# Kernel optimization log

Measured on AMD Instinct MI355X. Metric: run time of the kernel, lower is better.

Reference implementation:

```python
import jax, jax.numpy as jnp
import numpy as np

EPS = 1e-5
GROUPS = 8

def group_norm(x, gamma, beta):
    # x: [B,C,H,W], 8 groups
    B, C, H, W = x.shape
    xg = x.reshape(B, GROUPS, C // GROUPS, H, W)
    mu = jnp.mean(xg, axis=(2, 3, 4), keepdims=True)
    var = jnp.mean((xg - mu) ** 2, axis=(2, 3, 4), keepdims=True)
    xn = ((xg - mu) * jax.lax.rsqrt(var + EPS)).reshape(B, C, H, W)
    return xn * gamma[None, :, None, None] + beta[None, :, None, None]

def setup_inputs() -> dict:
    key = jax.random.key(0)
    ks = jax.random.split(key, 7)
    B, C, H, W = 4, 256, 64, 64
    x = jax.random.normal(ks[0], (B, C, H, W), dtype=jnp.float32)
    gamma = jnp.ones((C,), dtype=jnp.float32)
    beta = jnp.zeros((C,), dtype=jnp.float32)
    s = 1.0 / np.sqrt(C)
    w_qkv = jax.random.normal(ks[1], (3 * C, C), dtype=jnp.float32) * s
    b_qkv = jnp.zeros((3 * C,), dtype=jnp.float32)
    w_proj = jax.random.normal(ks[2], (C, C), dtype=jnp.float32) * s
    b_proj = jnp.zeros((C,), dtype=jnp.float32)
    return {"x": x, "gamma": gamma, "beta": beta, "w_qkv": w_qkv,
            "b_qkv": b_qkv, "w_proj": w_proj, "b_proj": b_proj}

def reference(x, gamma, beta, w_qkv, b_qkv, w_proj, b_proj):
    B, C, H, W = x.shape
    N = H * W
    h = group_norm(x, gamma, beta)
    # 1x1 conv == per-pixel matmul
    qkv = jnp.einsum('bchw,oc->bohw', h, w_qkv) + b_qkv[None, :, None, None]
    q, k, v = jnp.split(qkv, 3, axis=1)  # each [B,C,H,W]
    q = q.reshape(B, C, N).transpose(0, 2, 1)   # [B,N,C]
    k = k.reshape(B, C, N)                      # [B,C,N]
    v = v.reshape(B, C, N).transpose(0, 2, 1)   # [B,N,C]
    attn = jax.nn.softmax(jnp.einsum('bnc,bcm->bnm', q, k) / jnp.sqrt(jnp.float32(C)), axis=-1)
    out = jnp.einsum('bnm,bmc->bnc', attn, v)   # [B,N,C]
    out = out.transpose(0, 2, 1).reshape(B, C, H, W)
    proj = jnp.einsum('bchw,oc->bohw', out, w_proj) + b_proj[None, :, None, None]
    return x + proj
```

## Files before the change

### kernel.cpp

```cpp
#include <hip/hip_runtime.h>
#include <hip/hip_bf16.h>
#include <math.h>

#define B 4
#define C 256
#define G 8
#define N 4096
#define EPSV 1e-5f
#define SCALE 0.0625f

typedef __attribute__((ext_vector_type(8))) short short8;
typedef __attribute__((ext_vector_type(16))) float f32x16;
typedef unsigned short ushort_t;
typedef unsigned int uint_t;

__device__ __forceinline__ ushort_t f2bf(float f) {
    union { float f; uint_t u; } c; c.f = f;
    uint_t u = c.u;
    uint_t r = (u + 0x7FFFu + ((u >> 16) & 1u)) >> 16;
    return (ushort_t)r;
}
__device__ __forceinline__ float bf2f(ushort_t h) {
    union { uint_t u; float f; } c; c.u = ((uint_t)h) << 16;
    return c.f;
}
__device__ __forceinline__ uint_t pack2(float a, float b) {
    return (uint_t)f2bf(a) | ((uint_t)f2bf(b) << 16);
}
__device__ __forceinline__ uint_t cvtpk_bf16(float lo, float hi) {
    uint_t r;
    asm("v_cvt_pk_bf16_f32 %0, %1, %2" : "=v"(r) : "v"(lo), "v"(hi));
    return r;
}
__device__ __forceinline__ void gl_lds16(const void* g, void* l) {
    __builtin_amdgcn_global_load_lds(
        (const __attribute__((address_space(1))) void*)g,
        (__attribute__((address_space(3))) void*)l, 16, 0, 0);
}

__global__ __launch_bounds__(256) void wconv(const float* __restrict__ wq,
        const float* __restrict__ wp, ushort_t* __restrict__ wbf) {
    int idx = blockIdx.x*256 + threadIdx.x;
    #pragma unroll
    for (int p = 0; p < 4; p++) {
        int id = idx + p*16384;
        float4 v = (id < 49152) ? ((const float4*)wq)[id] : ((const float4*)wp)[id - 49152];
        uint2 pk; pk.x = pack2(v.x, v.y); pk.y = pack2(v.z, v.w);
        *(uint2*)&wbf[(size_t)id*4] = pk;
    }
}

__global__ __launch_bounds__(256) void gn_partial(const float* __restrict__ x,
                                                  float* __restrict__ partials) {
    int blk = blockIdx.x;
    int bg = blk >> 3;
    int part = blk & 7;
    const float4* xp4 = (const float4*)(x + (size_t)bg * (32 * N) + (size_t)part * (32 * N / 8));
    float s = 0.f, ss = 0.f;
    for (int i = threadIdx.x; i < 4096; i += 256) {
        float4 v = xp4[i];
        s  += v.x + v.y + v.z + v.w;
        ss += v.x*v.x + v.y*v.y + v.z*v.z + v.w*v.w;
    }
    __shared__ float rs[256], rss[256];
    rs[threadIdx.x] = s; rss[threadIdx.x] = ss;
    __syncthreads();
    for (int off = 128; off > 0; off >>= 1) {
        if (threadIdx.x < off) {
            rs[threadIdx.x]  += rs[threadIdx.x + off];
            rss[threadIdx.x] += rss[threadIdx.x + off];
        }
        __syncthreads();
    }
    if (threadIdx.x == 0) {
        partials[(bg*8 + part)*2]     = rs[0];
        partials[(bg*8 + part)*2 + 1] = rss[0];
    }
}

__global__ void gn_final(const float* __restrict__ partials, float* __restrict__ stats) {
    int t = threadIdx.x;
    if (t < 32) {
        float s = 0.f, ss = 0.f;
        for (int p = 0; p < 8; p++) {
            s  += partials[(t*8 + p)*2];
            ss += partials[(t*8 + p)*2 + 1];
        }
        const float inv = 1.f / 131072.f;
        float mu = s * inv;
        float var = fmaxf(ss * inv - mu*mu, 0.f);
        stats[t*2]     = mu;
        stats[t*2 + 1] = rsqrtf(var + EPSV);
    }
}

__global__ __launch_bounds__(256) void norm_bf16(const float* __restrict__ x,
        const float* __restrict__ gamma, const float* __restrict__ beta,
        const float* __restrict__ stats, ushort_t* __restrict__ hbf) {
    int b = blockIdx.z, c0 = blockIdx.y*64, n0 = blockIdx.x*64;
    int t = threadIdx.x;
    int cq = t >> 4, nq = t & 15;
    ushort_t hv[4][4];
    #pragma unroll
    for (int i = 0; i < 4; i++) {
        int c = c0 + cq*4 + i;
        int g = c >> 5;
        float mu = stats[(b*G+g)*2], rs = stats[(b*G+g)*2+1];
        float ga = gamma[c]*rs;
        float be = beta[c] - mu*ga;
        float4 v = *(const float4*)&x[((size_t)(b*C + c))*N + n0 + nq*4];
        hv[i][0] = f2bf(v.x*ga + be);
        hv[i][1] = f2bf(v.y*ga + be);
        hv[i][2] = f2bf(v.z*ga + be);
        hv[i][3] = f2bf(v.w*ga + be);
    }
    #pragma unroll
    for (int j = 0; j < 4; j++) {
        uint2 pk;
        pk.x = (uint_t)hv[0][j] | ((uint_t)hv[1][j]<<16);
        pk.y = (uint_t)hv[2][j] | ((uint_t)hv[3][j]<<16);
        *(uint2*)&hbf[((size_t)(b*N + n0 + nq*4 + j))*256 + c0 + cq*4] = pk;
    }
}

__global__ __launch_bounds__(256) void qkv_mfma(const ushort_t* __restrict__ hbf,
        const ushort_t* __restrict__ wbf, const float* __restrict__ bias,
        ushort_t* __restrict__ qbf, ushort_t* __restrict__ kbf, ushort_t* __restrict__ vblk) {
    int b = blockIdx.z, o0 = blockIdx.y*128, n0 = blockIdx.x*128;
    int tid = threadIdx.x;
    int w = tid>>6, l = tid&63, l31 = l&31, lh = l>>5;
    __shared__ short Ws[2][8192];
    __shared__ short Hs[2][8192];

    const ushort_t* wb = wbf + (size_t)o0*256;
    const ushort_t* hb = hbf + ((size_t)b*N + n0)*256;

    auto stage = [&](int bb, int c0) {
        #pragma unroll
        for (int q = 0; q < 4; q++) {
            int u0 = (q*4 + w)*64;
            int u  = u0 + l;
            int row = u & 127, ch = u >> 7;
            gl_lds16(wb + (size_t)row*256 + c0 + ch*8, &Ws[bb][u0*8]);
            gl_lds16(hb + (size_t)row*256 + c0 + ch*8, &Hs[bb][u0*8]);
        }
    };

    f32x16 acc[4];
    #pragma unroll
    for (int nf = 0; nf < 4; nf++)
        #pragma unroll
        for (int r = 0; r < 16; r++) acc[nf][r] = 0.f;

    stage(0, 0);
    __syncthreads();
    for (int t = 0; t < 4; t++) {
        int bb = t & 1;
        if (t < 3) stage(bb^1, (t+1)*64);
        short8 af[4];
        #pragma unroll
        for (int s = 0; s < 4; s++)
            af[s] = *(const short8*)&Ws[bb][((2*s+lh)*128 + w*32 + l31)*8];
        #pragma unroll
        for (int nf = 0; nf < 4; nf++) {
            #pragma unroll
            for (int s = 0; s < 4; s++) {
                short8 hf = *(const short8*)&Hs[bb][((2*s+lh)*128 + nf*32 + l31)*8];
                acc[nf] = __builtin_amdgcn_mfma_f32_32x32x16_bf16(af[s], hf, acc[nf], 0, 0, 0);
            }
        }
        __syncthreads();
    }

    int ow = o0 + w*32;
    float bv[16];
    #pragma unroll
    for (int r = 0; r < 16; r++) bv[r] = bias[ow + (r&3) + 8*(r>>2) + 4*lh];

    if (ow < 512) {
        ushort_t* dst = (ow < 256) ? qbf : kbf;
        int cb = ow & 255;
        float sc = (ow < 256) ? SCALE : 1.0f;
        #pragma unroll
        for (int nf = 0; nf < 4; nf++) {
            int n = n0 + nf*32 + l31;
            ushort_t* row = dst + ((size_t)(b*N + n))*256 + cb;
            #pragma unroll
            for (int rp = 0; rp < 8; rp++) {
                int r0 = rp*2;
                int cl = (r0&3) + 8*(r0>>2) + 4*lh;
                uint_t wd = cvtpk_bf16((acc[nf][r0]+bv[r0])*sc, (acc[nf][r0+1]+bv[r0+1])*sc);
                *(uint_t*)(row + cl) = wd;
            }
        }
    } else {
        int cb = ow - 512;
        #pragma unroll
        for (int nf = 0; nf < 4; nf++) {
            int n = n0 + nf*32 + l31;
            ushort_t* base = vblk + (size_t)b*1048576 + (size_t)(n>>5)*8192 + (size_t)cb*32 + (n&31);
            #pragma unroll
            for (int r = 0; r < 16; r++) {
                int cl = (r&3) + 8*(r>>2) + 4*lh;
                base[(size_t)cl*32] = f2bf(acc[nf][r] + bv[r]);
            }
        }
    }
}

__global__ __launch_bounds__(256, 1) void attn_mfma(const ushort_t* __restrict__ qbf,
        const ushort_t* __restrict__ kbf, const ushort_t* __restrict__ vblk,
        ushort_t* __restrict__ part, float* __restrict__ ml) {
    int f = blockIdx.x;
    int qt  = f >> 3;
    int b   = (f >> 1) & 3;
    int kvh = f & 1;
    constexpr int NT = 64;
    int w = threadIdx.x >> 6;
    int l = threadIdx.x & 63;
    int l31 = l & 31, lh = l >> 5;

    __shared__ short KV[3][2][8192];

    int qbase = qt*128 + w*32;
    short8 qf[16];
    {
        const ushort_t* qrow = qbf + ((size_t)(b*N + qbase + l31))*256;
        #pragma unroll
        for (int s = 0; s < 16; s++)
            qf[s] = *(const short8*)(qrow + s*16 + lh*8);
    }

    f32x16 ot[8];
    #pragma unroll
    for (int mc = 0; mc < 8; mc++)
        #pragma unroll
        for (int r = 0; r < 16; r++) ot[mc][r] = 0.f;
    float m = -INFINITY, lsum = 0.f;

    const char* kbase = (const char*)kbf + (size_t)(b*N)*512;
    const char* vbase = (const char*)vblk + (size_t)b*2097152;
    int m0base = kvh*2048;

    auto stage = [&](int slot, int t) {
        int m0 = m0base + t*32;
        const char* ks_ = kbase + ((size_t)(m0 + l31))*512;
        #pragma unroll
        for (int q = 0; q < 4; q++)
            gl_lds16(ks_ + (w*8 + q*2 + lh)*16, &KV[slot][0][(w*4+q)*512]);
        const char* vs_ = vbase + (size_t)(m0 >> 5)*16384 + w*16;
        #pragma unroll
        for (int q = 0; q < 4; q++)
            gl_lds16(vs_ + (q*64 + l)*64, &KV[slot][1][(w*4+q)*512]);
    };

    auto qk_issue = [&](int slot, f32x16& s0, f32x16& s1) {
        #pragma unroll
        for (int r = 0; r < 16; r++) { s0[r] = 0.f; s1[r] = 0.f; }
        const short* kb_ = &KV[slot][0][0];
        #pragma unroll
        for (int s = 0; s < 8; s++) {
            short8 ka = *(const short8*)(kb_ + ((size_t)((4*s   + lh)*32 + l31))*8);
            short8 kc = *(const short8*)(kb_ + ((size_t)((4*s+2 + lh)*32 + l31))*8);
            s0 = __builtin_amdgcn_mfma_f32_32x32x16_bf16(ka, qf[2*s],   s0, 0, 0, 0);
            s1 = __builtin_amdgcn_mfma_f32_32x32x16_bf16(kc, qf[2*s+1], s1, 0, 0, 0);
        }
    };

    auto body = [&](int t, f32x16& sc0, f32x16& sc1, f32x16& sn0, f32x16& sn1) {
        __syncthreads();
        int slot0 = t % 3;
        int slot1 = (t+1) % 3;
        int slot2 = (t+2) % 3;
        if (t+1 < NT) qk_issue(slot1, sn0, sn1);
        if (t+2 < NT) stage(slot2, t+2);

        float sv[16];
        #pragma unroll
        for (int r = 0; r < 16; r++) sv[r] = sc0[r] + sc1[r];
        float pmax = sv[0];
        #pragma unroll
        for (int r = 1; r < 16; r++) pmax = fmaxf(pmax, sv[r]);
        pmax = fmaxf(pmax, __shfl_xor(pmax, 32));
        if (!__all(pmax <= m + 8.0f)) {
            float mn = fmaxf(m, pmax);
            float fac = __expf(m - mn);
            m = mn;
            lsum *= fac;
            #pragma unroll
            for (int mc = 0; mc < 8; mc++)
                #pragma unroll
                for (int r = 0; r < 16; r++) ot[mc][r] *= fac;
        }
        float p[16]; float ls = 0.f;
        #pragma unroll
        for (int r = 0; r < 16; r++) { p[r] = __expf(sv[r] - m); ls += p[r]; }
        ls += __shfl_xor(ls, 32);
        lsum += ls;

        short8 pf0, pf1;
        {
            uint_t x0 = cvtpk_bf16(p[0], p[1]);
            uint_t y0 = cvtpk_bf16(p[4], p[5]);
            uint_t x1 = cvtpk_bf16(p[2], p[3]);
            uint_t y1 = cvtpk_bf16(p[6], p[7]);
            auto r0 = __builtin_amdgcn_permlane32_swap(x0, y0, false, false);
            auto r1 = __builtin_amdgcn_permlane32_swap(x1, y1, false, false);
            union { uint_t u[4]; short8 s8; } u_;
            u_.u[0] = r0[0]; u_.u[1] = r1[0]; u_.u[2] = r0[1]; u_.u[3] = r1[1];
            pf0 = u_.s8;
            uint_t x2 = cvtpk_bf16(p[8],  p[9]);
            uint_t y2 = cvtpk_bf16(p[12], p[13]);
            uint_t x3 = cvtpk_bf16(p[10], p[11]);
            uint_t y3 = cvtpk_bf16(p[14], p[15]);
            auto r2 = __builtin_amdgcn_permlane32_swap(x2, y2, false, false);
            auto r3 = __builtin_amdgcn_permlane32_swap(x3, y3, false, false);
            union { uint_t u[4]; short8 s8; } u2_;
            u2_.u[0] = r2[0]; u2_.u[1] = r3[0]; u2_.u[2] = r2[1]; u2_.u[3] = r3[1];
            pf1 = u2_.s8;
        }

        const short* vb_ = &KV[slot0][1][0];
        #pragma unroll
        for (int mc = 0; mc < 8; mc++) {
            short8 v0 = *(const short8*)(vb_ + ((size_t)((lh)*256   + mc*32 + l31))*8);
            short8 v1 = *(const short8*)(vb_ + ((size_t)((2+lh)*256 + mc*32 + l31))*8);
            ot[mc] = __builtin_amdgcn_mfma_f32_32x32x16_bf16(v0, pf0, ot[mc], 0, 0, 0);
            ot[mc] = __builtin_amdgcn_mfma_f32_32x32x16_bf16(v1, pf1, ot[mc], 0, 0, 0);
        }
    };

    f32x16 stA0, stA1, stB0, stB1;

    stage(0, 0);
    __syncthreads();
    qk_issue(0, stA0, stA1);
    stage(1, 1);

    for (int t = 0; t < NT; t += 2) {
        body(t,   stA0, stA1, stB0, stB1);
        body(t+1, stB0, stB1, stA0, stA1);
    }

    float invl = 1.f / lsum;
    ushort_t* pbase = part + (size_t)kvh*4194304 + ((size_t)(b*N + qbase + l31))*256;
    #pragma unroll
    for (int mc = 0; mc < 8; mc++)
        #pragma unroll
        for (int rp = 0; rp < 8; rp++) {
            int r0 = rp*2;
            uint_t wd = cvtpk_bf16(ot[mc][r0]*invl, ot[mc][r0+1]*invl);
            int c0 = (r0 & 3) + 8*(r0 >> 2) + 4*lh + 32*mc;
            *(uint_t*)(pbase + c0) = wd;
        }
    if (l < 32) {
        size_t row = (size_t)kvh*16384 + b*4096 + qbase + l;
        ml[row*2]     = m;
        ml[row*2 + 1] = lsum;
    }
}

__global__ __launch_bounds__(256) void attn_merge(const ushort_t* __restrict__ part,
        const float* __restrict__ ml, ushort_t* __restrict__ ob) {
    int t = blockIdx.x*256 + threadIdx.x;
    int row = t >> 5;
    int c8 = (t & 31) * 8;
    float m0 = ml[(size_t)row*2],           l0 = ml[(size_t)row*2 + 1];
    float m1 = ml[(size_t)(16384 + row)*2], l1 = ml[(size_t)(16384 + row)*2 + 1];
    float M = fmaxf(m0, m1);
    float w0 = __expf(m0 - M) * l0, w1 = __expf(m1 - M) * l1;
    float inv = 1.f / (w0 + w1);
    w0 *= inv; w1 *= inv;
    const ushort_t* p0 = part + (size_t)row*256 + c8;
    const ushort_t* p1 = p0 + 4194304;
    float o[8];
    #pragma unroll
    for (int e = 0; e < 8; e++) o[e] = w0*bf2f(p0[e]) + w1*bf2f(p1[e]);
    uint4 pk;
    pk.x = pack2(o[0], o[1]);
    pk.y = pack2(o[2], o[3]);
    pk.z = pack2(o[4], o[5]);
    pk.w = pack2(o[6], o[7]);
    *(uint4*)(ob + (size_t)row*256 + c8) = pk;
}

__global__ __launch_bounds__(256) void proj_mfma(const ushort_t* __restrict__ obf,
        const ushort_t* __restrict__ wpbf, const float* __restrict__ bp,
        const float* __restrict__ x, float* __restrict__ out) {
    int b = blockIdx.z, o0 = blockIdx.y*128, n0 = blockIdx.x*128;
    int tid = threadIdx.x;
    int w = tid>>6, l = tid&63, l31 = l&31, lh = l>>5;
    __shared__ short Ws[2][8192];
    __shared__ short Hs[2][8192];

    const ushort_t* wb = wpbf + (size_t)o0*256;
    const ushort_t* hb = obf + ((size_t)b*N + n0)*256;

    auto stage = [&](int bb, int c0) {
        #pragma unroll
        for (int q = 0; q < 4; q++) {
            int u0 = (q*4 + w)*64;
            int u  = u0 + l;
            int row = u & 127, ch = u >> 7;
            gl_lds16(wb + (size_t)row*256 + c0 + ch*8, &Ws[bb][u0*8]);
            gl_lds16(hb + (size_t)row*256 + c0 + ch*8, &Hs[bb][u0*8]);
        }
    };

    f32x16 acc[4];
    #pragma unroll
    for (int nf = 0; nf < 4; nf++)
        #pragma unroll
        for (int r = 0; r < 16; r++) acc[nf][r] = 0.f;

    stage(0, 0);
    __syncthreads();
    for (int t = 0; t < 4; t++) {
        int bb = t & 1;
        if (t < 3) stage(bb^1, (t+1)*64);
        short8 af[4];
        #pragma unroll
        for (int s = 0; s < 4; s++)
            af[s] = *(const short8*)&Ws[bb][((2*s+lh)*128 + w*32 + l31)*8];
        #pragma unroll
        for (int nf = 0; nf < 4; nf++) {
            #pragma unroll
            for (int s = 0; s < 4; s++) {
                short8 hf = *(const short8*)&Hs[bb][((2*s+lh)*128 + nf*32 + l31)*8];
                acc[nf] = __builtin_amdgcn_mfma_f32_32x32x16_bf16(af[s], hf, acc[nf], 0, 0, 0);
            }
        }
        __syncthreads();
    }

    int cw = o0 + w*32;
    float bv[16];
    #pragma unroll
    for (int r = 0; r < 16; r++) bv[r] = bp[cw + (r&3) + 8*(r>>2) + 4*lh];

    #pragma unroll
    for (int nf = 0; nf < 4; nf++) {
        int n = n0 + nf*32 + l31;
        #pragma unroll
        for (int r = 0; r < 16; r++) {
            int cl = (r&3) + 8*(r>>2) + 4*lh;
            size_t a = ((size_t)b*C + cw + cl)*N + n;
            out[a] = acc[nf][r] + bv[r] + x[a];
        }
    }
}

extern "C" void kernel_launch(void* const* d_in, const int* in_sizes, int n_in,
                              void* d_out, int out_size, void* d_ws, size_t ws_size,
                              hipStream_t stream) {
    const float* x      = (const float*)d_in[0];
    const float* gamma  = (const float*)d_in[1];
    const float* beta   = (const float*)d_in[2];
    const float* w_qkv  = (const float*)d_in[3];
    const float* b_qkv  = (const float*)d_in[4];
    const float* w_proj = (const float*)d_in[5];
    const float* b_proj = (const float*)d_in[6];
    float* out = (float*)d_out;
    char* wsb  = (char*)d_ws;

    const size_t MB = 1048576;
    ushort_t* qbf  = (ushort_t*)(wsb);
    ushort_t* kbf  = (ushort_t*)(wsb + 8*MB);
    ushort_t* vblk = (ushort_t*)(wsb + 16*MB);
    ushort_t* part = (ushort_t*)(wsb + 24*MB);
    ushort_t* hbf  = part;
    float*    ml   = (float*)  (wsb + 40*MB);
    ushort_t* ob   = (ushort_t*)(wsb + 40*MB + 524288);
    float* partials = (float*) (wsb + 48*MB + 524288);
    float* stats    = partials + 512;
    ushort_t* wbf  = (ushort_t*)(wsb + 48*MB + 524288 + 4096);

    wconv<<<dim3(64), dim3(256), 0, stream>>>(w_qkv, w_proj, wbf);
    gn_partial<<<dim3(256), dim3(256), 0, stream>>>(x, partials);
    gn_final<<<dim3(1), dim3(64), 0, stream>>>(partials, stats);
    norm_bf16<<<dim3(64, 4, 4), dim3(256), 0, stream>>>(x, gamma, beta, stats, hbf);
    qkv_mfma<<<dim3(32, 6, 4), dim3(256), 0, stream>>>(hbf, wbf, b_qkv, qbf, kbf, vblk);
    attn_mfma<<<dim3(256), dim3(256), 0, stream>>>(qbf, kbf, vblk, part, ml);
    attn_merge<<<dim3(2048), dim3(256), 0, stream>>>(part, ml, ob);
    proj_mfma<<<dim3(32, 2, 4), dim3(256), 0, stream>>>(ob, wbf + 196608, b_proj, x, out);
}
```

Measured before the change: 168.0 us.

## Write K and V in LDS-image tile layout so attention staging is contiguous

New measurement: 163.7 us. -2.6%, faster.

```diff
diff --git a/kernel.cpp b/kernel.cpp
--- a/kernel.cpp
+++ b/kernel.cpp
@@ -125,7 +125,7 @@
 
 __global__ __launch_bounds__(256) void qkv_mfma(const ushort_t* __restrict__ hbf,
         const ushort_t* __restrict__ wbf, const float* __restrict__ bias,
-        ushort_t* __restrict__ qbf, ushort_t* __restrict__ kbf, ushort_t* __restrict__ vblk) {
+        ushort_t* __restrict__ qbf, ushort_t* __restrict__ kimg, ushort_t* __restrict__ vimg) {
     int b = blockIdx.z, o0 = blockIdx.y*128, n0 = blockIdx.x*128;
     int tid = threadIdx.x;
     int w = tid>>6, l = tid&63, l31 = l&31, lh = l>>5;
@@ -177,39 +177,52 @@
     #pragma unroll
     for (int r = 0; r < 16; r++) bv[r] = bias[ow + (r&3) + 8*(r>>2) + 4*lh];
 
-    if (ow < 512) {
-        ushort_t* dst = (ow < 256) ? qbf : kbf;
-        int cb = ow & 255;
-        float sc = (ow < 256) ? SCALE : 1.0f;
+    if (ow < 256) {
         #pragma unroll
         for (int nf = 0; nf < 4; nf++) {
             int n = n0 + nf*32 + l31;
-            ushort_t* row = dst + ((size_t)(b*N + n))*256 + cb;
+            ushort_t* row = qbf + ((size_t)(b*N + n))*256 + ow;
             #pragma unroll
             for (int rp = 0; rp < 8; rp++) {
                 int r0 = rp*2;
                 int cl = (r0&3) + 8*(r0>>2) + 4*lh;
-                uint_t wd = cvtpk_bf16((acc[nf][r0]+bv[r0])*sc, (acc[nf][r0+1]+bv[r0+1])*sc);
+                uint_t wd = cvtpk_bf16((acc[nf][r0]+bv[r0])*SCALE, (acc[nf][r0+1]+bv[r0+1])*SCALE);
                 *(uint_t*)(row + cl) = wd;
             }
         }
+    } else if (ow < 512) {
+        int cb = ow - 256;
+        #pragma unroll
+        for (int nf = 0; nf < 4; nf++) {
+            int n = n0 + nf*32 + l31;
+            ushort_t* tbase = kimg + (size_t)b*1048576 + (size_t)(n>>5)*8192
+                            + (size_t)l31*8 + 4*lh;
+            #pragma unroll
+            for (int g = 0; g < 4; g++) {
+                uint2 pk;
+                pk.x = pack2(acc[nf][g*4+0]+bv[g*4+0], acc[nf][g*4+1]+bv[g*4+1]);
+                pk.y = pack2(acc[nf][g*4+2]+bv[g*4+2], acc[nf][g*4+3]+bv[g*4+3]);
+                *(uint2*)(tbase + (size_t)((cb>>3)+g)*256) = pk;
+            }
+        }
     } else {
         int cb = ow - 512;
         #pragma unroll
         for (int nf = 0; nf < 4; nf++) {
             int n = n0 + nf*32 + l31;
-            ushort_t* base = vblk + (size_t)b*1048576 + (size_t)(n>>5)*8192 + (size_t)cb*32 + (n&31);
+            ushort_t* tbase = vimg + (size_t)b*1048576 + (size_t)(n>>5)*8192
+                            + (size_t)(l31>>3)*2048 + (l31&7);
             #pragma unroll
             for (int r = 0; r < 16; r++) {
                 int cl = (r&3) + 8*(r>>2) + 4*lh;
-                base[(size_t)cl*32] = f2bf(acc[nf][r] + bv[r]);
+                tbase[(size_t)(cb+cl)*8] = f2bf(acc[nf][r] + bv[r]);
             }
         }
     }
 }
 
 __global__ __launch_bounds__(256, 1) void attn_mfma(const ushort_t* __restrict__ qbf,
-        const ushort_t* __restrict__ kbf, const ushort_t* __restrict__ vblk,
+        const ushort_t* __restrict__ kimg, const ushort_t* __restrict__ vimg,
         ushort_t* __restrict__ part, float* __restrict__ ml) {
     int f = blockIdx.x;
     int qt  = f >> 3;
@@ -238,20 +251,20 @@
         for (int r = 0; r < 16; r++) ot[mc][r] = 0.f;
     float m = -INFINITY, lsum = 0.f;
 
-    const char* kbase = (const char*)kbf + (size_t)(b*N)*512;
-    const char* vbase = (const char*)vblk + (size_t)b*2097152;
+    const char* kbase = (const char*)kimg + (size_t)b*2097152;
+    const char* vbase = (const char*)vimg + (size_t)b*2097152;
     int m0base = kvh*2048;
 
     auto stage = [&](int slot, int t) {
-        int m0 = m0base + t*32;
-        const char* ks_ = kbase + ((size_t)(m0 + l31))*512;
-        #pragma unroll
-        for (int q = 0; q < 4; q++)
-            gl_lds16(ks_ + (w*8 + q*2 + lh)*16, &KV[slot][0][(w*4+q)*512]);
-        const char* vs_ = vbase + (size_t)(m0 >> 5)*16384 + w*16;
-        #pragma unroll
-        for (int q = 0; q < 4; q++)
-            gl_lds16(vs_ + (q*64 + l)*64, &KV[slot][1][(w*4+q)*512]);
+        int tile = (m0base >> 5) + t;
+        const char* kt = kbase + (size_t)tile*16384;
+        const char* vt = vbase + (size_t)tile*16384;
+        #pragma unroll
+        for (int q = 0; q < 4; q++) {
+            int u0 = (w*4 + q)*64;
+            gl_lds16(kt + (u0 + l)*16, &KV[slot][0][u0*8]);
+            gl_lds16(vt + (u0 + l)*16, &KV[slot][1][u0*8]);
+        }
     };
 
     auto qk_issue = [&](int slot, f32x16& s0, f32x16& s1) {
@@ -465,8 +478,8 @@
 
     const size_t MB = 1048576;
     ushort_t* qbf  = (ushort_t*)(wsb);
-    ushort_t* kbf  = (ushort_t*)(wsb + 8*MB);
-    ushort_t* vblk = (ushort_t*)(wsb + 16*MB);
+    ushort_t* kimg = (ushort_t*)(wsb + 8*MB);
+    ushort_t* vimg = (ushort_t*)(wsb + 16*MB);
     ushort_t* part = (ushort_t*)(wsb + 24*MB);
     ushort_t* hbf  = part;
     float*    ml   = (float*)  (wsb + 40*MB);
@@ -479,8 +492,8 @@
     gn_partial<<<dim3(256), dim3(256), 0, stream>>>(x, partials);
     gn_final<<<dim3(1), dim3(64), 0, stream>>>(partials, stats);
     norm_bf16<<<dim3(64, 4, 4), dim3(256), 0, stream>>>(x, gamma, beta, stats, hbf);
-    qkv_mfma<<<dim3(32, 6, 4), dim3(256), 0, stream>>>(hbf, wbf, b_qkv, qbf, kbf, vblk);
-    attn_mfma<<<dim3(256), dim3(256), 0, stream>>>(qbf, kbf, vblk, part, ml);
+    qkv_mfma<<<dim3(32, 6, 4), dim3(256), 0, stream>>>(hbf, wbf, b_qkv, qbf, kimg, vimg);
+    attn_mfma<<<dim3(256), dim3(256), 0, stream>>>(qbf, kimg, vimg, part, ml);
     attn_merge<<<dim3(2048), dim3(256), 0, stream>>>(part, ml, ob);
     proj_mfma<<<dim3(32, 2, 4), dim3(256), 0, stream>>>(ob, wbf + 196608, b_proj, x, out);
 }
```
